# Optimization experiments

Measured on AMD Instinct MI355X. Metric: run time of the kernel, lower is better.

Reference implementation:

```python
import jax, jax.numpy as jnp
import numpy as np

B, S, D = 2, 2048, 1024
H = 16
HD = D // H  # 64
SCALE = HD ** -0.5
EPS = 1e-12  # F.normalize eps


def _rope_sin_cos(length, half, dtype):
    positions = jnp.arange(length, dtype=dtype)
    freqs = jnp.arange(half, dtype=dtype)
    inv_freq = 1.0 / 10000 ** (freqs / max(1, half))
    theta = jnp.einsum('s,f->sf', positions, inv_freq)  # [S, half]
    return jnp.sin(theta)[None, None], jnp.cos(theta)[None, None]  # [1,1,S,half]


def _rotate(x, sin, cos):
    # x: [B,H,S,HD]; interleaved even/odd rotation
    x_even = x[..., 0::2]
    x_odd = x[..., 1::2]
    r_even = x_even * cos - x_odd * sin
    r_odd = x_even * sin + x_odd * cos
    return jnp.stack([r_even, r_odd], axis=-1).reshape(x.shape)


def setup_inputs() -> dict:
    key = jax.random.key(0)
    k1, k2, k3 = jax.random.split(key, 3)
    tokens = jax.random.normal(k1, (B, S, D), dtype=jnp.float32)
    qkv_w = jax.random.normal(k2, (3 * D, D), dtype=jnp.float32) * (D ** -0.5)
    qkv_b = jnp.zeros((3 * D,), dtype=jnp.float32)
    out_w = jax.random.normal(k3, (D, D), dtype=jnp.float32) * (D ** -0.5)
    out_b = jnp.zeros((D,), dtype=jnp.float32)
    return {"tokens": tokens, "qkv_w": qkv_w, "qkv_b": qkv_b,
            "out_w": out_w, "out_b": out_b}


def reference(tokens, qkv_w, qkv_b, out_w, out_b):
    batch, length, _ = tokens.shape
    qkv = tokens @ qkv_w.T + qkv_b                       # [B,S,3D]
    qkv = qkv.reshape(batch, length, 3, H, HD)
    qkv = jnp.transpose(qkv, (0, 3, 1, 2, 4))            # [B,H,S,3,HD]
    q, k, v = qkv[..., 0, :], qkv[..., 1, :], qkv[..., 2, :]
    sin, cos = _rope_sin_cos(length, HD // 2, q.dtype)
    q = _rotate(q, sin, cos)
    k = _rotate(k, sin, cos)
    # QK L2-normalize (F.normalize: x / max(||x||, eps))
    q = q / jnp.maximum(jnp.linalg.norm(q, axis=-1, keepdims=True), EPS)
    k = k / jnp.maximum(jnp.linalg.norm(k, axis=-1, keepdims=True), EPS)
    scores = jnp.einsum('bhqd,bhkd->bhqk', q, k) * SCALE
    attn = jax.nn.softmax(scores, axis=-1)
    out = jnp.einsum('bhqk,bhkd->bhqd', attn, v)          # [B,H,S,HD]
    out = jnp.transpose(out, (0, 2, 1, 3)).reshape(batch, length, D)
    return out @ out_w.T + out_b
```

## Files before the change

kernel.cpp:

```cpp
#include <hip/hip_runtime.h>
#include <hip/hip_bf16.h>
#include <math.h>

#define B_ 2
#define S_ 2048
#define D_ 1024
#define H_ 16
#define HD_ 64
#define BHS (B_*H_*S_)
#define NROWS (B_*S_)

typedef __attribute__((ext_vector_type(8))) short bf16x8;
typedef __attribute__((ext_vector_type(4))) short bf16x4;
typedef __attribute__((ext_vector_type(4))) float f32x4;
typedef __attribute__((ext_vector_type(4))) int i32x4;

#ifdef __HIP_DEVICE_COMPILE__
#define EXP2(x) __builtin_amdgcn_exp2f(x)
#else
#define EXP2(x) exp2f(x)
#endif

#define MFMA32(a, b, c) __builtin_amdgcn_mfma_f32_16x16x32_bf16(a, b, c, 0, 0, 0)

#define SCALE_LOG2E 0.18033688011112043f

#define VMCNT(N) asm volatile("s_waitcnt vmcnt(" #N ")" ::: "memory")
#define SBAR() do { __builtin_amdgcn_s_barrier(); \
                    __builtin_amdgcn_sched_barrier(0); } while (0)
#define SCHED0() __builtin_amdgcn_sched_barrier(0)

__device__ __forceinline__ short f2bf(float x) {
  __hip_bfloat16 h = __float2bfloat16(x);
  return *reinterpret_cast<short*>(&h);
}
__device__ __forceinline__ int packbf_hu(float lo, float hi) {
  unsigned lb = __float_as_uint(lo) + 0x8000u;
  unsigned hb = __float_as_uint(hi) + 0x8000u;
  return (int)__builtin_amdgcn_perm(hb, lb, 0x07060302u);
}

__device__ __forceinline__ void gload_lds16(const short* g, short* l) {
  __builtin_amdgcn_global_load_lds(
      (const __attribute__((address_space(1))) void*)g,
      (__attribute__((address_space(3))) void*)l, 16, 0, 0);
}

__global__ __launch_bounds__(256) void prep(
    const float* __restrict__ tokens, const float* __restrict__ qkv_w,
    const float* __restrict__ out_w, short* __restrict__ tok_bf,
    short* __restrict__ qkvw_bf, short* __restrict__ outw_bf,
    float* __restrict__ tab) {
  const int i = blockIdx.x * 256 + threadIdx.x;
  const float* src;
  short* dst;
  int j;
  if (i < 524288) {
    src = tokens; dst = tok_bf; j = i;
  } else if (i < 917504) {
    src = qkv_w; dst = qkvw_bf; j = i - 524288;
  } else if (i < 1048576) {
    src = out_w; dst = outw_bf; j = i - 917504;
  } else if (i < 1056768) {
    const int e = (i - 1048576) * 8;
    const int s = e >> 5;
    const int f0 = e & 31;
#pragma unroll
    for (int k = 0; k < 8; k++) {
      const int f = f0 + k;
      const float theta = (float)s * exp2f(-(float)f * 0.41524101186092034f);
      float sn, cs;
      sincosf(theta, &sn, &cs);
      tab[(s * 32 + f) * 2] = sn;
      tab[(s * 32 + f) * 2 + 1] = cs;
    }
    return;
  } else {
    return;
  }
  const float4 a = *(const float4*)(src + (long)j * 8);
  const float4 b = *(const float4*)(src + (long)j * 8 + 4);
  short tmp[8] = {f2bf(a.x), f2bf(a.y), f2bf(a.z), f2bf(a.w),
                  f2bf(b.x), f2bf(b.y), f2bf(b.z), f2bf(b.w)};
  *(bf16x8*)(dst + (long)j * 8) = *(const bf16x8*)tmp;
}

__global__ __launch_bounds__(256) void qkv_mfma(
    const short* __restrict__ A, const short* __restrict__ W,
    const float* __restrict__ bias, const float* __restrict__ tab,
    short* __restrict__ qb, short* __restrict__ kb, short* __restrict__ vtb) {
  __shared__ short smem[32768];
  const int t = threadIdx.x;
  const int w = t >> 6;
  const int lane = t & 63;
  const int col = lane & 15;
  const int quad = lane >> 4;
  const int wm = w >> 1;
  const int wn = w & 1;
  const int bid = blockIdx.x;
  const int xcd = bid & 7;
  const int seq = bid >> 3;
  const int m0 = (seq / 3) * 128;
  const int n0 = (xcd * 3 + seq % 3) * 128;

  f32x4 acc[4][4] = {};

  auto stage = [&](short* As, short* Bs, int k0) {
#pragma unroll
    for (int i = 0; i < 4; i++) {
      const int c0 = i * 256 + w * 64;
      const int c = c0 + lane;
      const int row = c >> 3;
      const int gseg = (c & 7) ^ (row & 7);
      gload_lds16(&A[(m0 + row) * 1024 + k0 + gseg * 8], As + c0 * 8);
    }
#pragma unroll
    for (int i = 0; i < 4; i++) {
      const int c0 = i * 256 + w * 64;
      const int c = c0 + lane;
      const int row = c >> 3;
      const int gseg = (c & 7) ^ (row & 7);
      gload_lds16(&W[(n0 + row) * 1024 + k0 + gseg * 8], Bs + c0 * 8);
    }
  };

  auto compute = [&](const short* As, const short* Bs) {
#pragma unroll
    for (int half = 0; half < 2; half++) {
      bf16x8 af[4], bfr[4];
#pragma unroll
      for (int mt = 0; mt < 4; mt++) {
        const int m = wm * 64 + mt * 16 + col;
        af[mt] =
            *(const bf16x8*)&As[m * 64 + (((quad + half * 4) ^ (m & 7)) * 8)];
      }
#pragma unroll
      for (int nt = 0; nt < 4; nt++) {
        const int n = wn * 64 + nt * 16 + col;
        bfr[nt] =
            *(const bf16x8*)&Bs[n * 64 + (((quad + half * 4) ^ (n & 7)) * 8)];
      }
#pragma unroll
      for (int mt = 0; mt < 4; mt++)
#pragma unroll
        for (int nt = 0; nt < 4; nt++)
          acc[mt][nt] = MFMA32(af[mt], bfr[nt], acc[mt][nt]);
    }
  };

  short* As0 = smem;          short* Bs0 = smem + 8192;
  short* As1 = smem + 16384;  short* Bs1 = smem + 24576;

  stage(As0, Bs0, 0);
  for (int it = 0; it < 8; it++) {
    const int k = it * 128;
    VMCNT(0); SBAR();
    stage(As1, Bs1, k + 64);
    SCHED0();
    compute(As0, Bs0);
    VMCNT(0); SBAR();
    if (it < 7) stage(As0, Bs0, k + 128);
    SCHED0();
    compute(As1, Bs1);
  }
  __syncthreads();

  const int j_base = n0 + wn * 64;
  const int c = j_base >> 10;
  const int h = (j_base >> 6) & 15;
  float bi[4];
#pragma unroll
  for (int nt = 0; nt < 4; nt++) bi[nt] = bias[j_base + nt * 16 + col];

  if (c < 2) {
    short* dst = (c == 0) ? qb : kb;
    float* Tf = (float*)smem + w * 1088;
#pragma unroll
    for (int mt = 0; mt < 4; mt++) {
#pragma unroll
      for (int nt = 0; nt < 4; nt++)
#pragma unroll
        for (int r = 0; r < 4; r++)
          Tf[(quad * 4 + r) * 68 + nt * 16 + col] = acc[mt][nt][r] + bi[nt];
#pragma unroll
      for (int p = 0; p < 4; p++) {
        const int rloc = p * 4 + quad;
        const int n = m0 + wm * 64 + mt * 16 + rloc;
        const int bidx = n >> 11;
        const int s = n & 2047;
        const float4 xv = *(const float4*)&Tf[rloc * 68 + col * 4];
        const float4 tc = *(const float4*)&tab[s * 64 + col * 4];
        const float e0 = xv.x * tc.y - xv.y * tc.x;
        const float o0 = xv.x * tc.x + xv.y * tc.y;
        const float e1 = xv.z * tc.w - xv.w * tc.z;
        const float o1 = xv.z * tc.z + xv.w * tc.w;
        float ss = e0 * e0 + o0 * o0 + e1 * e1 + o1 * o1;
        ss += __shfl_xor(ss, 1, 64);
        ss += __shfl_xor(ss, 2, 64);
        ss += __shfl_xor(ss, 4, 64);
        ss += __shfl_xor(ss, 8, 64);
        float scl = 1.0f / fmaxf(sqrtf(ss), 1e-12f);
        if (c == 0) scl *= SCALE_LOG2E;
        int2 pk;
        pk.x = packbf_hu(e0 * scl, o0 * scl);
        pk.y = packbf_hu(e1 * scl, o1 * scl);
        *(int2*)&dst[((long)(bidx * 16 + h) * 2048 + s) * 64 + col * 4] = pk;
      }
    }
  } else {
    const int bidx = m0 >> 11;
    const int st = ((m0 & 2047) >> 6) + wm;
    short* vbase = vtb + ((long)(bidx * 16 + h) * 32 + st) * 4096;
#pragma unroll
    for (int mtp = 0; mtp < 2; mtp++)
#pragma unroll
      for (int ntq = 0; ntq < 4; ntq++) {
        int4 pk4;
        pk4.x = packbf_hu(acc[2 * mtp][ntq][0] + bi[ntq],
                          acc[2 * mtp][ntq][1] + bi[ntq]);
        pk4.y = packbf_hu(acc[2 * mtp][ntq][2] + bi[ntq],
                          acc[2 * mtp][ntq][3] + bi[ntq]);
        pk4.z = packbf_hu(acc[2 * mtp + 1][ntq][0] + bi[ntq],
                          acc[2 * mtp + 1][ntq][1] + bi[ntq]);
        pk4.w = packbf_hu(acc[2 * mtp + 1][ntq][2] + bi[ntq],
                          acc[2 * mtp + 1][ntq][3] + bi[ntq]);
        *(int4*)&vbase[(mtp * 4 + ntq) * 512 + quad * 128 + col * 8] = pk4;
      }
  }
}

__global__ __launch_bounds__(256) void attn_mfma(
    const short* __restrict__ qb,
    const short* __restrict__ kb,
    const short* __restrict__ vt,
    short* __restrict__ ob) {
  __shared__ __align__(16) char smem[65536];
  short* Ks = (short*)smem;
  short* Vs = Ks + 16384;
  const int t = threadIdx.x;
  const int w = t >> 6;
  const int grp = w >> 1;
  const int wl = w & 1;
  const int lane = t & 63;
  const int col = lane & 15;
  const int quad = lane >> 4;
  const int bh = blockIdx.x;
  const int q0 = blockIdx.y * 128;
  const long hb = (long)bh * S_ * 64;
  const short* kg = kb + hb;
  const short* vg = vt + (long)bh * 64 * S_;

  bf16x8 qa[4][2];
#pragma unroll
  for (int mt2 = 0; mt2 < 4; mt2++)
#pragma unroll
    for (int h = 0; h < 2; h++)
      qa[mt2][h] = *(const bf16x8*)&qb[hb +
          (long)(q0 + wl * 64 + mt2 * 16 + col) * 64 + h * 32 + quad * 8];

  const int tt = (wl << 6) | lane;
  int kofs[4];
#pragma unroll
  for (int i = 0; i < 4; i++) {
    const int cc = i * 128 + tt;
    kofs[i] = ((cc >> 7) * 16 + (cc & 15)) * 64 + ((cc >> 6) & 1) * 32 +
              ((cc >> 4) & 3) * 8;
  }

  short* KfL0 = Ks + grp * 4096;
  short* KfL1 = KfL0 + 8192;
  short* VfL0 = Vs + grp * 4096;
  short* VfL1 = VfL0 + 8192;

  f32x4 oacc[4][4] = {};
  f32x4 lacc[4] = {};
  const short oneb = 0x3F80;
  const bf16x8 ones8 = {oneb, oneb, oneb, oneb, oneb, oneb, oneb, oneb};

  auto stage = [&](short* KfL, short* VfL, int kt) {
    const short* kgp = kg + (long)kt * 64;
    const short* vgp = vg + (long)(kt >> 6) * 4096;
#pragma unroll
    for (int i = 0; i < 4; i++) {
      gload_lds16(kgp + kofs[i], KfL + i * 1024 + wl * 512);
      gload_lds16(vgp + (i * 128 + tt) * 8, VfL + i * 1024 + wl * 512);
    }
  };

  auto compute = [&](const short* KfL, const short* VfL) {
#pragma unroll
    for (int ntp = 0; ntp < 2; ntp++) {
      i32x4 pw[4];
#pragma unroll
      for (int half = 0; half < 2; half++) {
        const int nt = ntp * 2 + half;
        const bf16x8 ka0 =
            *(const bf16x8*)&KfL[nt * 1024 + quad * 128 + col * 8];
        const bf16x8 ka1 =
            *(const bf16x8*)&KfL[nt * 1024 + 512 + quad * 128 + col * 8];
#pragma unroll
        for (int mt2 = 0; mt2 < 4; mt2++) {
          f32x4 z = {0.f, 0.f, 0.f, 0.f};
          z = MFMA32(ka0, qa[mt2][0], z);
          z = MFMA32(ka1, qa[mt2][1], z);
          const float e0 = EXP2(z[0]);
          const float e1 = EXP2(z[1]);
          const float e2 = EXP2(z[2]);
          const float e3 = EXP2(z[3]);
          if (half == 0) {
            pw[mt2].x = packbf_hu(e0, e1);
            pw[mt2].y = packbf_hu(e2, e3);
          } else {
            pw[mt2].z = packbf_hu(e0, e1);
            pw[mt2].w = packbf_hu(e2, e3);
          }
        }
      }
      bf16x8 pb[4];
#pragma unroll
      for (int j = 0; j < 4; j++) {
        pb[j] = __builtin_bit_cast(bf16x8, pw[j]);
        lacc[j] = MFMA32(ones8, pb[j], lacc[j]);
      }
#pragma unroll
      for (int dt = 0; dt < 4; dt++) {
        const bf16x8 va = *(const bf16x8*)
            &VfL[(ntp * 4 + dt) * 512 + quad * 128 + col * 8];
#pragma unroll
        for (int j = 0; j < 4; j++)
          oacc[j][dt] = MFMA32(va, pb[j], oacc[j][dt]);
      }
    }
  };

  const int base = grp * 1024;
  stage(KfL0, VfL0, base);
  for (int it = 0; it < 8; it++) {
    const int kt0 = base + it * 128;
    VMCNT(0); SBAR();
    stage(KfL1, VfL1, kt0 + 64);
    SCHED0();
    compute(KfL0, VfL0);
    VMCNT(0); SBAR();
    if (it < 7) stage(KfL0, VfL0, kt0 + 128);
    SCHED0();
    compute(KfL1, VfL1);
  }
  __syncthreads();

  float* Ocomb = (float*)smem;
  float* lsumC = (float*)(smem + 34816);
  if (grp == 1) {
#pragma unroll
    for (int mt2 = 0; mt2 < 4; mt2++) {
      const int qloc = wl * 64 + mt2 * 16 + col;
      if (quad == 0) lsumC[qloc] = lacc[mt2][0];
#pragma unroll
      for (int dt = 0; dt < 4; dt++)
        *(f32x4*)&Ocomb[qloc * 68 + dt * 16 + quad * 4] = oacc[mt2][dt];
    }
  }
  __syncthreads();
  if (grp == 0) {
#pragma unroll
    for (int mt2 = 0; mt2 < 4; mt2++) {
      const int qloc = wl * 64 + mt2 * 16 + col;
      const float inv = 1.0f / (lacc[mt2][0] + lsumC[qloc]);
      short* orow = ob + hb + (long)(q0 + qloc) * 64;
#pragma unroll
      for (int dt = 0; dt < 4; dt++) {
        const float4 oc = *(const float4*)&Ocomb[qloc * 68 + dt * 16 + quad * 4];
        int2 pk;
        pk.x = packbf_hu((oacc[mt2][dt][0] + oc.x) * inv,
                         (oacc[mt2][dt][1] + oc.y) * inv);
        pk.y = packbf_hu((oacc[mt2][dt][2] + oc.z) * inv,
                         (oacc[mt2][dt][3] + oc.w) * inv);
        *(int2*)&orow[dt * 16 + quad * 4] = pk;
      }
    }
  }
}

__global__ __launch_bounds__(256) void out_mfma(
    const short* __restrict__ O, const short* __restrict__ W,
    const float* __restrict__ bias, float* __restrict__ out) {
  __shared__ short smem[16384];
  const int t = threadIdx.x;
  const int w = t >> 6;
  const int lane = t & 63;
  const int col = lane & 15;
  const int quad = lane >> 4;
  const int wm = w >> 1;
  const int wn = w & 1;
  const int bid = blockIdx.x;
  const int xcd = bid & 7;
  const int seq = bid >> 3;
  const int m0 = (seq >> 1) * 64;
  const int n0 = (xcd * 2 + (seq & 1)) * 64;

  f32x4 acc[2][2] = {};

  auto stage = [&](short* As, short* Bs, int k0) {
#pragma unroll
    for (int i = 0; i < 2; i++) {
      const int c0 = i * 256 + w * 64;
      const int c = c0 + lane;
      const int row = c >> 3;
      const int gseg = (c & 7) ^ (row & 7);
      const int n = m0 + row;
      const int bidx = n >> 11;
      const int s = n & 2047;
      const int kk = k0 + gseg * 8;
      gload_lds16(&O[((long)(bidx * 16 + (kk >> 6)) * 2048 + s) * 64 + (kk & 63)],
                  As + c0 * 8);
    }
#pragma unroll
    for (int i = 0; i < 2; i++) {
      const int c0 = i * 256 + w * 64;
      const int c = c0 + lane;
      const int row = c >> 3;
      const int gseg = (c & 7) ^ (row & 7);
      gload_lds16(&W[(n0 + row) * 1024 + k0 + gseg * 8], Bs + c0 * 8);
    }
  };

  auto compute = [&](const short* As, const short* Bs) {
#pragma unroll
    for (int half = 0; half < 2; half++) {
      bf16x8 af[2], bfr[2];
#pragma unroll
      for (int mt = 0; mt < 2; mt++) {
        const int m = wm * 32 + mt * 16 + col;
        af[mt] =
            *(const bf16x8*)&As[m * 64 + (((quad + half * 4) ^ (m & 7)) * 8)];
      }
#pragma unroll
      for (int nt = 0; nt < 2; nt++) {
        const int n = wn * 32 + nt * 16 + col;
        bfr[nt] =
            *(const bf16x8*)&Bs[n * 64 + (((quad + half * 4) ^ (n & 7)) * 8)];
      }
#pragma unroll
      for (int mt = 0; mt < 2; mt++)
#pragma unroll
        for (int nt = 0; nt < 2; nt++)
          acc[mt][nt] = MFMA32(af[mt], bfr[nt], acc[mt][nt]);
    }
  };

  short* As0 = smem;         short* Bs0 = smem + 4096;
  short* As1 = smem + 8192;  short* Bs1 = smem + 12288;

  stage(As0, Bs0, 0);
  for (int it = 0; it < 8; it++) {
    const int k = it * 128;
    VMCNT(0); SBAR();
    stage(As1, Bs1, k + 64);
    SCHED0();
    compute(As0, Bs0);
    VMCNT(0); SBAR();
    if (it < 7) stage(As0, Bs0, k + 128);
    SCHED0();
    compute(As1, Bs1);
  }

  float bi[2];
#pragma unroll
  for (int nt = 0; nt < 2; nt++) bi[nt] = bias[n0 + wn * 32 + nt * 16 + col];
#pragma unroll
  for (int mt = 0; mt < 2; mt++) {
#pragma unroll
    for (int r = 0; r < 4; r++) {
      const int n = m0 + wm * 32 + mt * 16 + quad * 4 + r;
#pragma unroll
      for (int nt = 0; nt < 2; nt++)
        out[(long)n * 1024 + n0 + wn * 32 + nt * 16 + col] =
            acc[mt][nt][r] + bi[nt];
    }
  }
}

extern "C" void kernel_launch(void* const* d_in, const int* in_sizes, int n_in,
                              void* d_out, int out_size, void* d_ws,
                              size_t ws_size, hipStream_t stream) {
  const float* tokens = (const float*)d_in[0];
  const float* qkv_w = (const float*)d_in[1];
  const float* qkv_b = (const float*)d_in[2];
  const float* out_w = (const float*)d_in[3];
  const float* out_b = (const float*)d_in[4];
  float* out = (float*)d_out;

  const size_t per = (size_t)BHS * HD_;
  float* tab = (float*)d_ws;
  short* tok_bf = (short*)(tab + 2048 * 64);
  short* qkvw_bf = tok_bf + per;
  short* outw_bf = qkvw_bf + 3 * per / 4;
  short* q_bf = outw_bf + per / 4;
  short* k_bf = q_bf + per;
  short* vt_bf = k_bf + per;
  short* O_bf = vt_bf + per;

  hipLaunchKernelGGL(prep, dim3(4128), dim3(256), 0, stream, tokens, qkv_w,
                     out_w, tok_bf, qkvw_bf, outw_bf, tab);
  hipLaunchKernelGGL(qkv_mfma, dim3(768), dim3(256), 0, stream, tok_bf,
                     qkvw_bf, qkv_b, tab, q_bf, k_bf, vt_bf);
  hipLaunchKernelGGL(attn_mfma, dim3(B_ * H_, S_ / 128), dim3(256), 0, stream,
                     q_bf, k_bf, vt_bf, O_bf);
  hipLaunchKernelGGL(out_mfma, dim3(1024), dim3(256), 0, stream, O_bf,
                     outw_bf, out_b, out);
}
```

Measured before the change: 196.2 us.

## Split attention key range across four wave groups with 512-thread blocks

The attention kernel now runs 512 threads per block and splits each query tile's key range across four wave groups instead of two. Each group handles 32-key steps. Groups 3 through 1 then reduce their partial outputs into shared memory one after another, and group 0 writes the final result. The row sum moves from a ones-vector MFMA to scalar adds with a shuffle reduction, and the P·V MFMAs run at raised wave priority. This is meant to add parallelism and latency hiding, at the cost of extra serialized reduction passes, more barriers and smaller tiles per step.

```diff
diff --git a/kernel.cpp b/kernel.cpp
--- a/kernel.cpp
+++ b/kernel.cpp
@@ -229,7 +229,7 @@
   }
 }
 
-__global__ __launch_bounds__(256) void attn_mfma(
+__global__ __launch_bounds__(512, 4) void attn_mfma(
     const short* __restrict__ qb,
     const short* __restrict__ kb,
     const short* __restrict__ vt,
@@ -259,113 +259,142 @@
           (long)(q0 + wl * 64 + mt2 * 16 + col) * 64 + h * 32 + quad * 8];
 
   const int tt = (wl << 6) | lane;
-  int kofs[4];
-#pragma unroll
-  for (int i = 0; i < 4; i++) {
+  int kofs[2];
+#pragma unroll
+  for (int i = 0; i < 2; i++) {
     const int cc = i * 128 + tt;
     kofs[i] = ((cc >> 7) * 16 + (cc & 15)) * 64 + ((cc >> 6) & 1) * 32 +
               ((cc >> 4) & 3) * 8;
   }
 
-  short* KfL0 = Ks + grp * 4096;
+  short* KfL0 = Ks + grp * 2048;
   short* KfL1 = KfL0 + 8192;
-  short* VfL0 = Vs + grp * 4096;
+  short* VfL0 = Vs + grp * 2048;
   short* VfL1 = VfL0 + 8192;
 
   f32x4 oacc[4][4] = {};
-  f32x4 lacc[4] = {};
-  const short oneb = 0x3F80;
-  const bf16x8 ones8 = {oneb, oneb, oneb, oneb, oneb, oneb, oneb, oneb};
+  float sacc[4] = {0.f, 0.f, 0.f, 0.f};
 
   auto stage = [&](short* KfL, short* VfL, int kt) {
     const short* kgp = kg + (long)kt * 64;
-    const short* vgp = vg + (long)(kt >> 6) * 4096;
-#pragma unroll
-    for (int i = 0; i < 4; i++) {
+    const short* vgp = vg + (long)(kt >> 6) * 4096 + ((kt >> 5) & 1) * 2048;
+#pragma unroll
+    for (int i = 0; i < 2; i++) {
       gload_lds16(kgp + kofs[i], KfL + i * 1024 + wl * 512);
       gload_lds16(vgp + (i * 128 + tt) * 8, VfL + i * 1024 + wl * 512);
     }
   };
 
   auto compute = [&](const short* KfL, const short* VfL) {
-#pragma unroll
-    for (int ntp = 0; ntp < 2; ntp++) {
-      i32x4 pw[4];
-#pragma unroll
-      for (int half = 0; half < 2; half++) {
-        const int nt = ntp * 2 + half;
-        const bf16x8 ka0 =
-            *(const bf16x8*)&KfL[nt * 1024 + quad * 128 + col * 8];
-        const bf16x8 ka1 =
-            *(const bf16x8*)&KfL[nt * 1024 + 512 + quad * 128 + col * 8];
-#pragma unroll
-        for (int mt2 = 0; mt2 < 4; mt2++) {
-          f32x4 z = {0.f, 0.f, 0.f, 0.f};
-          z = MFMA32(ka0, qa[mt2][0], z);
-          z = MFMA32(ka1, qa[mt2][1], z);
-          const float e0 = EXP2(z[0]);
-          const float e1 = EXP2(z[1]);
-          const float e2 = EXP2(z[2]);
-          const float e3 = EXP2(z[3]);
-          if (half == 0) {
-            pw[mt2].x = packbf_hu(e0, e1);
-            pw[mt2].y = packbf_hu(e2, e3);
-          } else {
-            pw[mt2].z = packbf_hu(e0, e1);
-            pw[mt2].w = packbf_hu(e2, e3);
-          }
+    i32x4 pw[4];
+#pragma unroll
+    for (int nt = 0; nt < 2; nt++) {
+      const bf16x8 ka0 = *(const bf16x8*)&KfL[nt * 1024 + quad * 128 + col * 8];
+      const bf16x8 ka1 =
+          *(const bf16x8*)&KfL[nt * 1024 + 512 + quad * 128 + col * 8];
+#pragma unroll
+      for (int mt2 = 0; mt2 < 4; mt2++) {
+        f32x4 z = {0.f, 0.f, 0.f, 0.f};
+        z = MFMA32(ka0, qa[mt2][0], z);
+        z = MFMA32(ka1, qa[mt2][1], z);
+        const float e0 = EXP2(z[0]);
+        const float e1 = EXP2(z[1]);
+        const float e2 = EXP2(z[2]);
+        const float e3 = EXP2(z[3]);
+        sacc[mt2] += (e0 + e1) + (e2 + e3);
+        if (nt == 0) {
+          pw[mt2].x = packbf_hu(e0, e1);
+          pw[mt2].y = packbf_hu(e2, e3);
+        } else {
+          pw[mt2].z = packbf_hu(e0, e1);
+          pw[mt2].w = packbf_hu(e2, e3);
         }
       }
-      bf16x8 pb[4];
-#pragma unroll
-      for (int j = 0; j < 4; j++) {
-        pb[j] = __builtin_bit_cast(bf16x8, pw[j]);
-        lacc[j] = MFMA32(ones8, pb[j], lacc[j]);
-      }
-#pragma unroll
-      for (int dt = 0; dt < 4; dt++) {
-        const bf16x8 va = *(const bf16x8*)
-            &VfL[(ntp * 4 + dt) * 512 + quad * 128 + col * 8];
-#pragma unroll
-        for (int j = 0; j < 4; j++)
-          oacc[j][dt] = MFMA32(va, pb[j], oacc[j][dt]);
-      }
-    }
+    }
+    __builtin_amdgcn_s_setprio(1);
+#pragma unroll
+    for (int dt = 0; dt < 4; dt++) {
+      const bf16x8 va =
+          *(const bf16x8*)&VfL[dt * 512 + quad * 128 + col * 8];
+#pragma unroll
+      for (int mt2 = 0; mt2 < 4; mt2++)
+        oacc[mt2][dt] =
+            MFMA32(va, __builtin_bit_cast(bf16x8, pw[mt2]), oacc[mt2][dt]);
+    }
+    __builtin_amdgcn_s_setprio(0);
   };
 
-  const int base = grp * 1024;
+  const int base = grp * 512;
   stage(KfL0, VfL0, base);
   for (int it = 0; it < 8; it++) {
-    const int kt0 = base + it * 128;
+    const int kt0 = base + it * 64;
     VMCNT(0); SBAR();
-    stage(KfL1, VfL1, kt0 + 64);
+    stage(KfL1, VfL1, kt0 + 32);
     SCHED0();
     compute(KfL0, VfL0);
     VMCNT(0); SBAR();
-    if (it < 7) stage(KfL0, VfL0, kt0 + 128);
+    if (it < 7) stage(KfL0, VfL0, kt0 + 64);
     SCHED0();
     compute(KfL1, VfL1);
   }
+
+  float sred[4];
+#pragma unroll
+  for (int mt2 = 0; mt2 < 4; mt2++) {
+    float ss = sacc[mt2];
+    ss += __shfl_xor(ss, 16, 64);
+    ss += __shfl_xor(ss, 32, 64);
+    sred[mt2] = ss;
+  }
+
   __syncthreads();
 
   float* Ocomb = (float*)smem;
   float* lsumC = (float*)(smem + 34816);
-  if (grp == 1) {
+  if (grp == 3) {
 #pragma unroll
     for (int mt2 = 0; mt2 < 4; mt2++) {
       const int qloc = wl * 64 + mt2 * 16 + col;
-      if (quad == 0) lsumC[qloc] = lacc[mt2][0];
+      if (quad == 0) lsumC[qloc] = sred[mt2];
 #pragma unroll
       for (int dt = 0; dt < 4; dt++)
         *(f32x4*)&Ocomb[qloc * 68 + dt * 16 + quad * 4] = oacc[mt2][dt];
     }
   }
   __syncthreads();
-  if (grp == 0) {
+  if (grp == 2) {
 #pragma unroll
     for (int mt2 = 0; mt2 < 4; mt2++) {
       const int qloc = wl * 64 + mt2 * 16 + col;
-      const float inv = 1.0f / (lacc[mt2][0] + lsumC[qloc]);
+      if (quad == 0) lsumC[qloc] += sred[mt2];
+#pragma unroll
+      for (int dt = 0; dt < 4; dt++) {
+        f32x4 v = *(const f32x4*)&Ocomb[qloc * 68 + dt * 16 + quad * 4];
+        v += oacc[mt2][dt];
+        *(f32x4*)&Ocomb[qloc * 68 + dt * 16 + quad * 4] = v;
+      }
+    }
+  }
+  __syncthreads();
+  if (grp == 1) {
+#pragma unroll
+    for (int mt2 = 0; mt2 < 4; mt2++) {
+      const int qloc = wl * 64 + mt2 * 16 + col;
+      if (quad == 0) lsumC[qloc] += sred[mt2];
+#pragma unroll
+      for (int dt = 0; dt < 4; dt++) {
+        f32x4 v = *(const f32x4*)&Ocomb[qloc * 68 + dt * 16 + quad * 4];
+        v += oacc[mt2][dt];
+        *(f32x4*)&Ocomb[qloc * 68 + dt * 16 + quad * 4] = v;
+      }
+    }
+  }
+  __syncthreads();
+  if (grp == 0) {
+#pragma unroll
+    for (int mt2 = 0; mt2 < 4; mt2++) {
+      const int qloc = wl * 64 + mt2 * 16 + col;
+      const float inv = 1.0f / (sred[mt2] + lsumC[qloc]);
       short* orow = ob + hb + (long)(q0 + qloc) * 64;
 #pragma unroll
       for (int dt = 0; dt < 4; dt++) {
@@ -504,7 +533,7 @@
                      out_w, tok_bf, qkvw_bf, outw_bf, tab);
   hipLaunchKernelGGL(qkv_mfma, dim3(768), dim3(256), 0, stream, tok_bf,
                      qkvw_bf, qkv_b, tab, q_bf, k_bf, vt_bf);
-  hipLaunchKernelGGL(attn_mfma, dim3(B_ * H_, S_ / 128), dim3(256), 0, stream,
+  hipLaunchKernelGGL(attn_mfma, dim3(B_ * H_, S_ / 128), dim3(512), 0, stream,
                      q_bf, k_bf, vt_bf, O_bf);
   hipLaunchKernelGGL(out_mfma, dim3(1024), dim3(256), 0, stream, O_bf,
                      outw_bf, out_b, out);
```

Result: slower. 345.6 us (+76.1%).
